# Kernel optimization log

Measured on AMD Instinct MI355X. Metric: run time of the kernel, lower is better.

The kernel has to match this reference:

```python
import jax, jax.numpy as jnp
import numpy as np

B, Hh, Ww, C = 4, 64, 64, 64


def setup_inputs() -> dict:
    key = jax.random.key(0)
    ks = jax.random.split(key, 5)
    scale = 1.0 / np.sqrt(C)
    return {
        "x": jax.random.normal(ks[0], (B, Hh, Ww, C), dtype=jnp.float32),
        "Wq": jax.random.normal(ks[1], (C, C), dtype=jnp.float32) * scale,
        "bq": jnp.zeros((C,), dtype=jnp.float32),
        "Wk": jax.random.normal(ks[2], (C, C), dtype=jnp.float32) * scale,
        "bk": jnp.zeros((C,), dtype=jnp.float32),
        "Wv": jax.random.normal(ks[3], (C, C), dtype=jnp.float32) * scale,
        "bv": jnp.zeros((C,), dtype=jnp.float32),
        "gamma": jax.random.normal(ks[4], (1,), dtype=jnp.float32) * 0.05,
    }


def reference(x, Wq, bq, Wk, bk, Wv, bv, gamma):
    b, h, w, c = x.shape
    n = h * w
    # 1x1 convs == per-pixel dense projections
    q = (jnp.einsum('bhwc,cf->bhwf', x, Wq) + bq).reshape(b, n, c)
    k = (jnp.einsum('bhwc,cf->bhwf', x, Wk) + bk).reshape(b, n, c)
    v = (jnp.einsum('bhwc,cf->bhwf', x, Wv) + bv).reshape(b, n, c)
    # energy[b, i, j] = <q_i, k_j>; no scaling, softmax over last axis (j)
    energy = jnp.einsum('bic,bjc->bij', q, k)
    attn = jax.nn.softmax(energy, axis=-1)
    # original: transpose(matmul(value^T, attention)) -> out[b,n,c] = sum_m attn[b,m,n] * v[b,m,c]
    out = jnp.einsum('bmn,bmc->bnc', attn, v)
    out = out.reshape(b, h, w, c)
    return gamma * out + x
```

## Files before the change

### kernel.cpp

```cpp
#include <hip/hip_runtime.h>
#include <hip/hip_bf16.h>


typedef __attribute__((ext_vector_type(8))) short short8;
typedef __attribute__((ext_vector_type(4))) float f32x4;
typedef __attribute__((ext_vector_type(4))) unsigned int u32x4;
typedef __attribute__((ext_vector_type(2))) unsigned int u32x2;

#define DEV static __device__ __forceinline__

DEV unsigned short f2bf(float f) {
    __hip_bfloat16 h = __float2bfloat16(f);
    return __builtin_bit_cast(unsigned short, h);
}
DEV unsigned int pack2(float lo, float hi) {
    return (unsigned int)f2bf(lo) | ((unsigned int)f2bf(hi) << 16);
}
DEV f32x4 MFMA(short8 a, short8 b, f32x4 c) {
    return __builtin_amdgcn_mfma_f32_16x16x32_bf16(a, b, c, 0, 0, 0);
}

#define OFF_Q    0u
#define OFF_K    2097152u
#define OFF_VT   4194304u
#define OFF_WT   6291456u
#define OFF_S    6316032u
#define OFF_RINV 6381568u

__global__ __launch_bounds__(256) void k0z(const float* __restrict__ Wq,
                                           const float* __restrict__ Wk,
                                           const float* __restrict__ Wv,
                                           unsigned short* __restrict__ wt,
                                           float* __restrict__ sbuf) {
    int e = blockIdx.x * 256 + threadIdx.x;
    sbuf[e] = 0.0f;
    if (e < 3 * 4096) {
        int w3 = e >> 12, rem = e & 4095, f = rem >> 6, c = rem & 63;
        const float* W = (w3 == 0) ? Wq : (w3 == 1) ? Wk : Wv;
        wt[e] = f2bf(W[c * 64 + f]);
    }
}

__global__ __launch_bounds__(256) void k1_proj(const float* __restrict__ x,
                                               const unsigned short* __restrict__ wt,
                                               const float* __restrict__ bq,
                                               const float* __restrict__ bk,
                                               const float* __restrict__ bv,
                                               unsigned short* __restrict__ qg,
                                               unsigned short* __restrict__ kg,
                                               unsigned short* __restrict__ vtg) {
    __shared__ __align__(16) char XT[8192];
    __shared__ __align__(16) char WT[24576];
    __shared__ __align__(16) char VTILE[9216];
    int t = threadIdx.x, blk = blockIdx.x;

    {
        int m = t >> 2, q4 = t & 3;
        const f32x4* xs = (const f32x4*)(x + (size_t)(blk * 64 + m) * 64 + q4 * 16);
        f32x4 fa = xs[0], fbv = xs[1], fc = xs[2], fd = xs[3];
        u32x4 u0 = { pack2(fa[0],fa[1]), pack2(fa[2],fa[3]), pack2(fbv[0],fbv[1]), pack2(fbv[2],fbv[3]) };
        u32x4 u1 = { pack2(fc[0],fc[1]), pack2(fc[2],fc[3]), pack2(fd[0],fd[1]), pack2(fd[2],fd[3]) };
        int sw = (m & 7) << 4;
        *(u32x4*)(XT + m * 128 + ((q4 * 32) ^ sw)) = u0;
        *(u32x4*)(XT + m * 128 + ((q4 * 32 + 16) ^ sw)) = u1;
    }
    for (int w3 = 0; w3 < 3; ++w3) {
        int f = t >> 2, q4 = t & 3;
        const u32x4* s = (const u32x4*)(wt + w3 * 4096 + f * 64 + q4 * 16);
        u32x4 u0 = s[0], u1 = s[1];
        int sw = (f & 7) << 4;
        *(u32x4*)(WT + w3 * 8192 + f * 128 + ((q4 * 32) ^ sw)) = u0;
        *(u32x4*)(WT + w3 * 8192 + f * 128 + ((q4 * 32 + 16) ^ sw)) = u1;
    }
    __syncthreads();

    int lane = t & 63, wid = t >> 6, g = lane >> 4, ln = lane & 15;
    int arow = wid * 16 + ln;
    short8 a0 = *(const short8*)(XT + arow * 128 + ((16 * g) ^ ((arow & 7) << 4)));
    short8 a1 = *(const short8*)(XT + arow * 128 + ((64 + 16 * g) ^ ((arow & 7) << 4)));

    for (int w3 = 0; w3 < 3; ++w3) {
        const char* wtile = WT + w3 * 8192;
        const float* bias = (w3 == 0) ? bq : (w3 == 1) ? bk : bv;
        #pragma unroll
        for (int fb = 0; fb < 4; ++fb) {
            int frow = fb * 16 + ln;
            short8 b0 = *(const short8*)(wtile + frow * 128 + ((16 * g) ^ ((frow & 7) << 4)));
            short8 b1 = *(const short8*)(wtile + frow * 128 + ((64 + 16 * g) ^ ((frow & 7) << 4)));
            f32x4 acc = {0.f, 0.f, 0.f, 0.f};
            acc = MFMA(a0, b0, acc);
            acc = MFMA(a1, b1, acc);
            float bval = bias[frow];
            if (w3 < 2) {
                unsigned short* dst = (w3 == 0) ? qg : kg;
                int gr = blk * 64 + wid * 16 + 4 * g;
                #pragma unroll
                for (int r = 0; r < 4; ++r)
                    dst[(size_t)(gr + r) * 64 + frow] = f2bf(acc[r] + bval);
            } else {
                unsigned short* vt = (unsigned short*)VTILE;
                int mloc = wid * 16 + 4 * g;
                #pragma unroll
                for (int r = 0; r < 4; ++r)
                    vt[frow * 72 + mloc + r] = f2bf(acc[r] + bval);
            }
        }
    }
    __syncthreads();
    {
        int f = t >> 2, mq = t & 3;
        u32x4 u0 = *(const u32x4*)(VTILE + f * 144 + mq * 32);
        u32x4 u1 = *(const u32x4*)(VTILE + f * 144 + mq * 32 + 16);
        int b = blk >> 6, n0 = (blk & 63) * 64;
        unsigned short* dst = vtg + (size_t)b * 262144 + f * 4096 + n0 + mq * 16;
        *(u32x4*)(dst) = u0;
        *(u32x4*)(dst + 8) = u1;
    }
}

__global__ __launch_bounds__(256) void k2_rowsum(const unsigned short* __restrict__ qg,
                                                 const unsigned short* __restrict__ kg,
                                                 float* __restrict__ sbuf) {
    __shared__ __align__(16) char QT[8192];
    __shared__ __align__(16) char KT[8192];
    int t = threadIdx.x, blk = blockIdx.x;
    int b = blk >> 8, ns = (blk >> 6) & 3, mb = blk & 63;
    int m0 = mb * 64, nbase = ns * 1024;
    int row = t >> 2, q4 = t & 3;
    int sw = (row & 7) << 4;

    {
        const u32x4* s = (const u32x4*)(qg + (size_t)(b * 4096 + m0 + row) * 64 + q4 * 16);
        u32x4 u0 = s[0], u1 = s[1];
        *(u32x4*)(QT + row * 128 + ((q4 * 32) ^ sw)) = u0;
        *(u32x4*)(QT + row * 128 + ((q4 * 32 + 16) ^ sw)) = u1;
    }
    u32x4 pf0, pf1;
    {
        const u32x4* ks = (const u32x4*)(kg + (size_t)(b * 4096 + nbase + row) * 64 + q4 * 16);
        pf0 = ks[0]; pf1 = ks[1];
    }
    __syncthreads();

    int lane = t & 63, wid = t >> 6, g = lane >> 4, ln = lane & 15;
    int arow = wid * 16 + ln;
    short8 a0 = *(const short8*)(QT + arow * 128 + ((16 * g) ^ ((arow & 7) << 4)));
    short8 a1 = *(const short8*)(QT + arow * 128 + ((64 + 16 * g) ^ ((arow & 7) << 4)));

    float acc0 = 0.f, acc1 = 0.f, acc2 = 0.f, acc3 = 0.f;
    for (int nc = 0; nc < 16; ++nc) {
        *(u32x4*)(KT + row * 128 + ((q4 * 32) ^ sw)) = pf0;
        *(u32x4*)(KT + row * 128 + ((q4 * 32 + 16) ^ sw)) = pf1;
        __syncthreads();
        if (nc < 15) {
            const u32x4* ks = (const u32x4*)(kg + (size_t)(b * 4096 + nbase + (nc + 1) * 64 + row) * 64 + q4 * 16);
            pf0 = ks[0]; pf1 = ks[1];
        }
        #pragma unroll
        for (int j = 0; j < 4; ++j) {
            int brow = j * 16 + ln;
            short8 b0 = *(const short8*)(KT + brow * 128 + ((16 * g) ^ ((brow & 7) << 4)));
            short8 b1 = *(const short8*)(KT + brow * 128 + ((64 + 16 * g) ^ ((brow & 7) << 4)));
            f32x4 e = {0.f, 0.f, 0.f, 0.f};
            e = MFMA(a0, b0, e);
            e = MFMA(a1, b1, e);
            acc0 += __expf(e[0]); acc1 += __expf(e[1]);
            acc2 += __expf(e[2]); acc3 += __expf(e[3]);
        }
        __syncthreads();
    }
    #pragma unroll
    for (int msk = 1; msk < 16; msk <<= 1) {
        acc0 += __shfl_xor(acc0, msk);
        acc1 += __shfl_xor(acc1, msk);
        acc2 += __shfl_xor(acc2, msk);
        acc3 += __shfl_xor(acc3, msk);
    }
    if (ln == 0) {
        float* base = sbuf + b * 4096 + m0 + wid * 16 + 4 * g;
        unsafeAtomicAdd(base + 0, acc0);
        unsafeAtomicAdd(base + 1, acc1);
        unsafeAtomicAdd(base + 2, acc2);
        unsafeAtomicAdd(base + 3, acc3);
    }
}

__global__ __launch_bounds__(256) void r2_init(const float* __restrict__ sbuf,
                                               float* __restrict__ rinv,
                                               const float* __restrict__ x,
                                               float* __restrict__ outp) {
    int tid = blockIdx.x * 256 + threadIdx.x;
    if (tid < 16384) rinv[tid] = 1.0f / sbuf[tid];
    f32x4 v = *(const f32x4*)(x + 4 * (size_t)tid);
    *(f32x4*)(outp + 4 * (size_t)tid) = v;
}

__global__ __launch_bounds__(256) void k3_out(const unsigned short* __restrict__ qg,
                                              const unsigned short* __restrict__ kg,
                                              const unsigned short* __restrict__ vtg,
                                              const float* __restrict__ rinv,
                                              const float* __restrict__ gamma,
                                              float* __restrict__ outp) {
    __shared__ __align__(16) char KT[8192];
    __shared__ __align__(16) char QT[8192];
    __shared__ __align__(16) char VT[8192];
    __shared__ __align__(16) char PL[8192];
    int t = threadIdx.x, blk = blockIdx.x;
    int b = blk >> 8, ms = (blk >> 6) & 3, nb = blk & 63;
    int n0 = nb * 64, mbase = ms * 1024;
    int row = t >> 2, q4 = t & 3;
    int sw = (row & 7) << 4;

    {
        const u32x4* s = (const u32x4*)(kg + (size_t)(b * 4096 + n0 + row) * 64 + q4 * 16);
        u32x4 u0 = s[0], u1 = s[1];
        *(u32x4*)(KT + row * 128 + ((q4 * 32) ^ sw)) = u0;
        *(u32x4*)(KT + row * 128 + ((q4 * 32 + 16) ^ sw)) = u1;
    }
    u32x4 qpf0, qpf1, vpf0, vpf1;
    {
        const u32x4* qs = (const u32x4*)(qg + (size_t)(b * 4096 + mbase + row) * 64 + q4 * 16);
        qpf0 = qs[0]; qpf1 = qs[1];
        const unsigned short* vs = vtg + (size_t)b * 262144 + row * 4096 + mbase + q4 * 16;
        vpf0 = *(const u32x4*)(vs);
        vpf1 = *(const u32x4*)(vs + 8);
    }
    __syncthreads();

    int lane = t & 63, wid = t >> 6, g = lane >> 4, ln = lane & 15;
    int krow = wid * 16 + ln;
    short8 kb0 = *(const short8*)(KT + krow * 128 + ((16 * g) ^ ((krow & 7) << 4)));
    short8 kb1 = *(const short8*)(KT + krow * 128 + ((64 + 16 * g) ^ ((krow & 7) << 4)));

    f32x4 z = {0.f, 0.f, 0.f, 0.f};
    f32x4 oacc[4] = {z, z, z, z};
    char* pbase = PL + wid * 2048;
    int psw = (ln & 7) << 4;
    const float* rblk = rinv + b * 4096 + mbase;

    for (int mc = 0; mc < 16; ++mc) {
        {
            *(u32x4*)(QT + row * 128 + ((q4 * 32) ^ sw)) = qpf0;
            *(u32x4*)(QT + row * 128 + ((q4 * 32 + 16) ^ sw)) = qpf1;
            *(u32x4*)(VT + row * 128 + ((q4 * 32) ^ sw)) = vpf0;
            *(u32x4*)(VT + row * 128 + ((q4 * 32 + 16) ^ sw)) = vpf1;
        }
        __syncthreads();
        if (mc < 15) {
            int m1 = mbase + (mc + 1) * 64;
            const u32x4* qs = (const u32x4*)(qg + (size_t)(b * 4096 + m1 + row) * 64 + q4 * 16);
            qpf0 = qs[0]; qpf1 = qs[1];
            const unsigned short* vs = vtg + (size_t)b * 262144 + row * 4096 + m1 + q4 * 16;
            vpf0 = *(const u32x4*)(vs);
            vpf1 = *(const u32x4*)(vs + 8);
        }
        const float* rp = rblk + mc * 64;
        #pragma unroll
        for (int s = 0; s < 4; ++s) {
            int qrow = 16 * s + ln;
            int qsw = (qrow & 7) << 4;
            short8 as0 = *(const short8*)(QT + qrow * 128 + ((16 * g) ^ qsw));
            short8 as1 = *(const short8*)(QT + qrow * 128 + ((64 + 16 * g) ^ qsw));
            f32x4 e = {0.f, 0.f, 0.f, 0.f};
            e = MFMA(as0, kb0, e);
            e = MFMA(as1, kb1, e);
            f32x4 rv = *(const f32x4*)(rp + 16 * s + 4 * g);
            float p0 = __expf(e[0]) * rv[0];
            float p1 = __expf(e[1]) * rv[1];
            float p2 = __expf(e[2]) * rv[2];
            float p3 = __expf(e[3]) * rv[3];
            u32x2 pu = { pack2(p0, p1), pack2(p2, p3) };
            *(u32x2*)(pbase + ln * 128 + ((32 * s + 8 * g) ^ psw)) = pu;
        }
        short8 pa0 = *(const short8*)(pbase + ln * 128 + ((16 * g) ^ psw));
        short8 pa1 = *(const short8*)(pbase + ln * 128 + ((64 + 16 * g) ^ psw));
        #pragma unroll
        for (int fb = 0; fb < 4; ++fb) {
            int crow = fb * 16 + ln;
            int csw = (crow & 7) << 4;
            short8 vb0 = *(const short8*)(VT + crow * 128 + ((16 * g) ^ csw));
            short8 vb1 = *(const short8*)(VT + crow * 128 + ((64 + 16 * g) ^ csw));
            oacc[fb] = MFMA(pa0, vb0, oacc[fb]);
            oacc[fb] = MFMA(pa1, vb1, oacc[fb]);
        }
        __syncthreads();
    }

    float gm = gamma[0];
    int nrow = b * 4096 + n0 + wid * 16 + 4 * g;
    #pragma unroll
    for (int fb = 0; fb < 4; ++fb) {
        #pragma unroll
        for (int r = 0; r < 4; ++r) {
            int idx = (nrow + r) * 64 + fb * 16 + ln;
            unsafeAtomicAdd(outp + idx, gm * oacc[fb][r]);
        }
    }
}

extern "C" void kernel_launch(void* const* d_in, const int* in_sizes, int n_in,
                              void* d_out, int out_size, void* d_ws, size_t ws_size,
                              hipStream_t stream) {
    const float* x  = (const float*)d_in[0];
    const float* Wq = (const float*)d_in[1];
    const float* bq = (const float*)d_in[2];
    const float* Wk = (const float*)d_in[3];
    const float* bk = (const float*)d_in[4];
    const float* Wv = (const float*)d_in[5];
    const float* bv = (const float*)d_in[6];
    const float* gm = (const float*)d_in[7];
    char* ws = (char*)d_ws;
    float* outp = (float*)d_out;

    unsigned short* qg  = (unsigned short*)(ws + OFF_Q);
    unsigned short* kg  = (unsigned short*)(ws + OFF_K);
    unsigned short* vtg = (unsigned short*)(ws + OFF_VT);
    unsigned short* wt  = (unsigned short*)(ws + OFF_WT);
    float* sbuf         = (float*)(ws + OFF_S);
    float* rinv         = (float*)(ws + OFF_RINV);

    k0z<<<64, 256, 0, stream>>>(Wq, Wk, Wv, wt, sbuf);
    k1_proj<<<256, 256, 0, stream>>>(x, wt, bq, bk, bv, qg, kg, vtg);
    k2_rowsum<<<1024, 256, 0, stream>>>(qg, kg, sbuf);
    r2_init<<<1024, 256, 0, stream>>>(sbuf, rinv, x, outp);
    k3_out<<<1024, 256, 0, stream>>>(qg, kg, vtg, rinv, gm, outp);
}
```

Baseline: 136.3 us.

## Fold log2e into Q, use exp2 with log-normalizer bias, restructure attention kernels

Folds log2(e) into the Q weights and bias, so the softmax exponentials become native exp2. The reciprocal row sum becomes a -log2 term that seeds the MFMA accumulator, which removes the per-element multiply. The projection kernel is split across three times as many blocks, one per weight matrix. The rowsum and output kernels get finer m/n splits, double-buffered smaller LDS tiles and occupancy hints. The output kernel also switches the P·V product to 16x16x16 MFMA fed straight from registers instead of an LDS round trip. The risks are more atomic-add traffic from twice as many blocks, more loop iterations with barriers, and bf16 precision changes from folding the scale into Q.

```diff
diff --git a/kernel.cpp b/kernel.cpp
--- a/kernel.cpp
+++ b/kernel.cpp
@@ -3,11 +3,13 @@
 
 
 typedef __attribute__((ext_vector_type(8))) short short8;
+typedef __attribute__((ext_vector_type(4))) short short4b;
 typedef __attribute__((ext_vector_type(4))) float f32x4;
 typedef __attribute__((ext_vector_type(4))) unsigned int u32x4;
 typedef __attribute__((ext_vector_type(2))) unsigned int u32x2;
 
 #define DEV static __device__ __forceinline__
+#define LOG2E 1.4426950408889634f
 
 DEV unsigned short f2bf(float f) {
     __hip_bfloat16 h = __float2bfloat16(f);
@@ -16,8 +18,26 @@
 DEV unsigned int pack2(float lo, float hi) {
     return (unsigned int)f2bf(lo) | ((unsigned int)f2bf(hi) << 16);
 }
-DEV f32x4 MFMA(short8 a, short8 b, f32x4 c) {
+DEV f32x4 MFMA32(short8 a, short8 b, f32x4 c) {
     return __builtin_amdgcn_mfma_f32_16x16x32_bf16(a, b, c, 0, 0, 0);
+}
+DEV f32x4 MFMA16(short4b a, short4b b, f32x4 c) {
+#if __has_builtin(__builtin_amdgcn_mfma_f32_16x16x16_bf16)
+    return __builtin_amdgcn_mfma_f32_16x16x16_bf16(a, b, c, 0, 0, 0);
+#elif __has_builtin(__builtin_amdgcn_mfma_f32_16x16x16bf16_1k)
+    return __builtin_amdgcn_mfma_f32_16x16x16bf16_1k(a, b, c, 0, 0, 0);
+#else
+    f32x4 d = c;
+    asm volatile("v_mfma_f32_16x16x16_bf16 %0, %1, %2, %0" : "+v"(d) : "v"(a), "v"(b));
+    return d;
+#endif
+}
+DEV float EXP2(float x) {
+#if __has_builtin(__builtin_amdgcn_exp2f)
+    return __builtin_amdgcn_exp2f(x);
+#else
+    return exp2f(x);
+#endif
 }
 
 #define OFF_Q    0u
@@ -25,7 +45,7 @@
 #define OFF_VT   4194304u
 #define OFF_WT   6291456u
 #define OFF_S    6316032u
-#define OFF_RINV 6381568u
+#define OFF_LR   6381568u
 
 __global__ __launch_bounds__(256) void k0z(const float* __restrict__ Wq,
                                            const float* __restrict__ Wk,
@@ -37,7 +57,8 @@
     if (e < 3 * 4096) {
         int w3 = e >> 12, rem = e & 4095, f = rem >> 6, c = rem & 63;
         const float* W = (w3 == 0) ? Wq : (w3 == 1) ? Wk : Wv;
-        wt[e] = f2bf(W[c * 64 + f]);
+        float s = (w3 == 0) ? LOG2E : 1.0f;
+        wt[e] = f2bf(W[c * 64 + f] * s);
     }
 }
 
@@ -50,27 +71,28 @@
                                                unsigned short* __restrict__ kg,
                                                unsigned short* __restrict__ vtg) {
     __shared__ __align__(16) char XT[8192];
-    __shared__ __align__(16) char WT[24576];
+    __shared__ __align__(16) char WT1[8192];
     __shared__ __align__(16) char VTILE[9216];
     int t = threadIdx.x, blk = blockIdx.x;
+    int w3 = blk >> 8, rb = blk & 255;
 
     {
         int m = t >> 2, q4 = t & 3;
-        const f32x4* xs = (const f32x4*)(x + (size_t)(blk * 64 + m) * 64 + q4 * 16);
-        f32x4 fa = xs[0], fbv = xs[1], fc = xs[2], fd = xs[3];
-        u32x4 u0 = { pack2(fa[0],fa[1]), pack2(fa[2],fa[3]), pack2(fbv[0],fbv[1]), pack2(fbv[2],fbv[3]) };
+        const f32x4* xs = (const f32x4*)(x + (size_t)(rb * 64 + m) * 64 + q4 * 16);
+        f32x4 fa = xs[0], f2 = xs[1], fc = xs[2], fd = xs[3];
+        u32x4 u0 = { pack2(fa[0],fa[1]), pack2(fa[2],fa[3]), pack2(f2[0],f2[1]), pack2(f2[2],f2[3]) };
         u32x4 u1 = { pack2(fc[0],fc[1]), pack2(fc[2],fc[3]), pack2(fd[0],fd[1]), pack2(fd[2],fd[3]) };
         int sw = (m & 7) << 4;
         *(u32x4*)(XT + m * 128 + ((q4 * 32) ^ sw)) = u0;
         *(u32x4*)(XT + m * 128 + ((q4 * 32 + 16) ^ sw)) = u1;
     }
-    for (int w3 = 0; w3 < 3; ++w3) {
+    {
         int f = t >> 2, q4 = t & 3;
         const u32x4* s = (const u32x4*)(wt + w3 * 4096 + f * 64 + q4 * 16);
         u32x4 u0 = s[0], u1 = s[1];
         int sw = (f & 7) << 4;
-        *(u32x4*)(WT + w3 * 8192 + f * 128 + ((q4 * 32) ^ sw)) = u0;
-        *(u32x4*)(WT + w3 * 8192 + f * 128 + ((q4 * 32 + 16) ^ sw)) = u1;
+        *(u32x4*)(WT1 + f * 128 + ((q4 * 32) ^ sw)) = u0;
+        *(u32x4*)(WT1 + f * 128 + ((q4 * 32 + 16) ^ sw)) = u1;
     }
     __syncthreads();
 
@@ -78,67 +100,65 @@
     int arow = wid * 16 + ln;
     short8 a0 = *(const short8*)(XT + arow * 128 + ((16 * g) ^ ((arow & 7) << 4)));
     short8 a1 = *(const short8*)(XT + arow * 128 + ((64 + 16 * g) ^ ((arow & 7) << 4)));
-
-    for (int w3 = 0; w3 < 3; ++w3) {
-        const char* wtile = WT + w3 * 8192;
-        const float* bias = (w3 == 0) ? bq : (w3 == 1) ? bk : bv;
-        #pragma unroll
-        for (int fb = 0; fb < 4; ++fb) {
-            int frow = fb * 16 + ln;
-            short8 b0 = *(const short8*)(wtile + frow * 128 + ((16 * g) ^ ((frow & 7) << 4)));
-            short8 b1 = *(const short8*)(wtile + frow * 128 + ((64 + 16 * g) ^ ((frow & 7) << 4)));
-            f32x4 acc = {0.f, 0.f, 0.f, 0.f};
-            acc = MFMA(a0, b0, acc);
-            acc = MFMA(a1, b1, acc);
-            float bval = bias[frow];
-            if (w3 < 2) {
-                unsigned short* dst = (w3 == 0) ? qg : kg;
-                int gr = blk * 64 + wid * 16 + 4 * g;
-                #pragma unroll
-                for (int r = 0; r < 4; ++r)
-                    dst[(size_t)(gr + r) * 64 + frow] = f2bf(acc[r] + bval);
-            } else {
-                unsigned short* vt = (unsigned short*)VTILE;
-                int mloc = wid * 16 + 4 * g;
-                #pragma unroll
-                for (int r = 0; r < 4; ++r)
-                    vt[frow * 72 + mloc + r] = f2bf(acc[r] + bval);
-            }
-        }
-    }
-    __syncthreads();
-    {
+    const float* bias = (w3 == 0) ? bq : (w3 == 1) ? bk : bv;
+    float bscale = (w3 == 0) ? LOG2E : 1.0f;
+
+    #pragma unroll
+    for (int fb = 0; fb < 4; ++fb) {
+        int frow = fb * 16 + ln;
+        short8 b0 = *(const short8*)(WT1 + frow * 128 + ((16 * g) ^ ((frow & 7) << 4)));
+        short8 b1 = *(const short8*)(WT1 + frow * 128 + ((64 + 16 * g) ^ ((frow & 7) << 4)));
+        f32x4 acc = {0.f, 0.f, 0.f, 0.f};
+        acc = MFMA32(a0, b0, acc);
+        acc = MFMA32(a1, b1, acc);
+        float bval = bias[frow] * bscale;
+        if (w3 < 2) {
+            unsigned short* dst = (w3 == 0) ? qg : kg;
+            int gr = rb * 64 + wid * 16 + 4 * g;
+            #pragma unroll
+            for (int r = 0; r < 4; ++r)
+                dst[(size_t)(gr + r) * 64 + frow] = f2bf(acc[r] + bval);
+        } else {
+            unsigned short* vt = (unsigned short*)VTILE;
+            int mloc = wid * 16 + 4 * g;
+            #pragma unroll
+            for (int r = 0; r < 4; ++r)
+                vt[frow * 72 + mloc + r] = f2bf(acc[r] + bval);
+        }
+    }
+    if (w3 == 2) {
+        __syncthreads();
         int f = t >> 2, mq = t & 3;
         u32x4 u0 = *(const u32x4*)(VTILE + f * 144 + mq * 32);
         u32x4 u1 = *(const u32x4*)(VTILE + f * 144 + mq * 32 + 16);
-        int b = blk >> 6, n0 = (blk & 63) * 64;
+        int b = rb >> 6, n0 = (rb & 63) * 64;
         unsigned short* dst = vtg + (size_t)b * 262144 + f * 4096 + n0 + mq * 16;
         *(u32x4*)(dst) = u0;
         *(u32x4*)(dst + 8) = u1;
     }
 }
 
-__global__ __launch_bounds__(256) void k2_rowsum(const unsigned short* __restrict__ qg,
-                                                 const unsigned short* __restrict__ kg,
-                                                 float* __restrict__ sbuf) {
+__global__ __launch_bounds__(256, 8) void k2_rowsum(const unsigned short* __restrict__ qg,
+                                                    const unsigned short* __restrict__ kg,
+                                                    float* __restrict__ sbuf) {
     __shared__ __align__(16) char QT[8192];
-    __shared__ __align__(16) char KT[8192];
+    __shared__ __align__(16) char KT2[2][4096];
     int t = threadIdx.x, blk = blockIdx.x;
-    int b = blk >> 8, ns = (blk >> 6) & 3, mb = blk & 63;
-    int m0 = mb * 64, nbase = ns * 1024;
-    int row = t >> 2, q4 = t & 3;
-    int sw = (row & 7) << 4;
-
-    {
+    int b = blk >> 9, ns = (blk >> 6) & 7, mb = blk & 63;
+    int m0 = mb * 64, nbase = ns * 512;
+
+    {
+        int row = t >> 2, q4 = t & 3, sw = (row & 7) << 4;
         const u32x4* s = (const u32x4*)(qg + (size_t)(b * 4096 + m0 + row) * 64 + q4 * 16);
         u32x4 u0 = s[0], u1 = s[1];
         *(u32x4*)(QT + row * 128 + ((q4 * 32) ^ sw)) = u0;
         *(u32x4*)(QT + row * 128 + ((q4 * 32 + 16) ^ sw)) = u1;
     }
-    u32x4 pf0, pf1;
-    {
-        const u32x4* ks = (const u32x4*)(kg + (size_t)(b * 4096 + nbase + row) * 64 + q4 * 16);
-        pf0 = ks[0]; pf1 = ks[1];
+    int srow = t >> 3, sb = t & 7, ssw = (srow & 7) << 4;
+    const unsigned short* kbase = kg + (size_t)(b * 4096 + nbase) * 64;
+    {
+        u32x4 u = *(const u32x4*)(kbase + srow * 64 + sb * 8);
+        *(u32x4*)(KT2[0] + srow * 128 + ((sb * 16) ^ ssw)) = u;
     }
     __syncthreads();
 
@@ -148,26 +168,27 @@
     short8 a1 = *(const short8*)(QT + arow * 128 + ((64 + 16 * g) ^ ((arow & 7) << 4)));
 
     float acc0 = 0.f, acc1 = 0.f, acc2 = 0.f, acc3 = 0.f;
+    int buf = 0;
+    u32x4 pf;
     for (int nc = 0; nc < 16; ++nc) {
-        *(u32x4*)(KT + row * 128 + ((q4 * 32) ^ sw)) = pf0;
-        *(u32x4*)(KT + row * 128 + ((q4 * 32 + 16) ^ sw)) = pf1;
+        if (nc < 15)
+            pf = *(const u32x4*)(kbase + (size_t)((nc + 1) * 32 + srow) * 64 + sb * 8);
+        const char* kt = KT2[buf];
+        #pragma unroll
+        for (int j = 0; j < 2; ++j) {
+            int brow = j * 16 + ln, bsw = (brow & 7) << 4;
+            short8 kb0 = *(const short8*)(kt + brow * 128 + ((16 * g) ^ bsw));
+            short8 kb1 = *(const short8*)(kt + brow * 128 + ((64 + 16 * g) ^ bsw));
+            f32x4 e = {0.f, 0.f, 0.f, 0.f};
+            e = MFMA32(a0, kb0, e);
+            e = MFMA32(a1, kb1, e);
+            acc0 += EXP2(e[0]); acc1 += EXP2(e[1]);
+            acc2 += EXP2(e[2]); acc3 += EXP2(e[3]);
+        }
+        if (nc < 15)
+            *(u32x4*)(KT2[buf ^ 1] + srow * 128 + ((sb * 16) ^ ssw)) = pf;
         __syncthreads();
-        if (nc < 15) {
-            const u32x4* ks = (const u32x4*)(kg + (size_t)(b * 4096 + nbase + (nc + 1) * 64 + row) * 64 + q4 * 16);
-            pf0 = ks[0]; pf1 = ks[1];
-        }
-        #pragma unroll
-        for (int j = 0; j < 4; ++j) {
-            int brow = j * 16 + ln;
-            short8 b0 = *(const short8*)(KT + brow * 128 + ((16 * g) ^ ((brow & 7) << 4)));
-            short8 b1 = *(const short8*)(KT + brow * 128 + ((64 + 16 * g) ^ ((brow & 7) << 4)));
-            f32x4 e = {0.f, 0.f, 0.f, 0.f};
-            e = MFMA(a0, b0, e);
-            e = MFMA(a1, b1, e);
-            acc0 += __expf(e[0]); acc1 += __expf(e[1]);
-            acc2 += __expf(e[2]); acc3 += __expf(e[3]);
-        }
-        __syncthreads();
+        buf ^= 1;
     }
     #pragma unroll
     for (int msk = 1; msk < 16; msk <<= 1) {
@@ -186,115 +207,97 @@
 }
 
 __global__ __launch_bounds__(256) void r2_init(const float* __restrict__ sbuf,
-                                               float* __restrict__ rinv,
+                                               float* __restrict__ lrbuf,
                                                const float* __restrict__ x,
                                                float* __restrict__ outp) {
     int tid = blockIdx.x * 256 + threadIdx.x;
-    if (tid < 16384) rinv[tid] = 1.0f / sbuf[tid];
+    if (tid < 16384) lrbuf[tid] = -__log2f(sbuf[tid]);
     f32x4 v = *(const f32x4*)(x + 4 * (size_t)tid);
     *(f32x4*)(outp + 4 * (size_t)tid) = v;
 }
 
-__global__ __launch_bounds__(256) void k3_out(const unsigned short* __restrict__ qg,
-                                              const unsigned short* __restrict__ kg,
-                                              const unsigned short* __restrict__ vtg,
-                                              const float* __restrict__ rinv,
-                                              const float* __restrict__ gamma,
-                                              float* __restrict__ outp) {
+__global__ __launch_bounds__(256, 8) void k3_out(const unsigned short* __restrict__ qg,
+                                                 const unsigned short* __restrict__ kg,
+                                                 const unsigned short* __restrict__ vtg,
+                                                 const float* __restrict__ lrbuf,
+                                                 const float* __restrict__ gamma,
+                                                 float* __restrict__ outp) {
     __shared__ __align__(16) char KT[8192];
-    __shared__ __align__(16) char QT[8192];
-    __shared__ __align__(16) char VT[8192];
-    __shared__ __align__(16) char PL[8192];
+    __shared__ __align__(16) char QT2[2][2048];
+    __shared__ __align__(16) char VT2[2][2560];
     int t = threadIdx.x, blk = blockIdx.x;
-    int b = blk >> 8, ms = (blk >> 6) & 3, nb = blk & 63;
-    int n0 = nb * 64, mbase = ms * 1024;
-    int row = t >> 2, q4 = t & 3;
-    int sw = (row & 7) << 4;
-
-    {
+    int b = blk >> 9, ms = (blk >> 6) & 7, nb = blk & 63;
+    int n0 = nb * 64, mbase = ms * 512;
+
+    {
+        int row = t >> 2, q4 = t & 3, sw = (row & 7) << 4;
         const u32x4* s = (const u32x4*)(kg + (size_t)(b * 4096 + n0 + row) * 64 + q4 * 16);
         u32x4 u0 = s[0], u1 = s[1];
         *(u32x4*)(KT + row * 128 + ((q4 * 32) ^ sw)) = u0;
         *(u32x4*)(KT + row * 128 + ((q4 * 32 + 16) ^ sw)) = u1;
     }
-    u32x4 qpf0, qpf1, vpf0, vpf1;
-    {
-        const u32x4* qs = (const u32x4*)(qg + (size_t)(b * 4096 + mbase + row) * 64 + q4 * 16);
-        qpf0 = qs[0]; qpf1 = qs[1];
-        const unsigned short* vs = vtg + (size_t)b * 262144 + row * 4096 + mbase + q4 * 16;
-        vpf0 = *(const u32x4*)(vs);
-        vpf1 = *(const u32x4*)(vs + 8);
-    }
+    int qrow = t >> 4, qh = t & 15;
+    int vc = t >> 2, vq = t & 3;
+    int qssw = (qrow & 7) << 4;
+    const unsigned short* qbase = qg + (size_t)(b * 4096 + mbase) * 64;
+    const unsigned short* vbase = vtg + (size_t)b * 262144 + (size_t)vc * 4096 + mbase;
+    {
+        u32x2 qu = *(const u32x2*)(qbase + qrow * 64 + qh * 4);
+        *(u32x2*)(QT2[0] + qrow * 128 + ((qh * 8) ^ qssw)) = qu;
+        u32x2 vu = *(const u32x2*)(vbase + vq * 4);
+        *(u32x2*)(VT2[0] + vc * 40 + vq * 8) = vu;
+    }
+    int lane = t & 63, wid = t >> 6, g = lane >> 4, ln = lane & 15;
+    const float* lrb = lrbuf + b * 4096 + mbase + 4 * g;
+    f32x4 lcur = *(const f32x4*)(lrb);
     __syncthreads();
 
-    int lane = t & 63, wid = t >> 6, g = lane >> 4, ln = lane & 15;
-    int krow = wid * 16 + ln;
-    short8 kb0 = *(const short8*)(KT + krow * 128 + ((16 * g) ^ ((krow & 7) << 4)));
-    short8 kb1 = *(const short8*)(KT + krow * 128 + ((64 + 16 * g) ^ ((krow & 7) << 4)));
+    int krow = wid * 16 + ln, ksw = (krow & 7) << 4;
+    short8 kb0 = *(const short8*)(KT + krow * 128 + ((16 * g) ^ ksw));
+    short8 kb1 = *(const short8*)(KT + krow * 128 + ((64 + 16 * g) ^ ksw));
 
     f32x4 z = {0.f, 0.f, 0.f, 0.f};
     f32x4 oacc[4] = {z, z, z, z};
-    char* pbase = PL + wid * 2048;
-    int psw = (ln & 7) << 4;
-    const float* rblk = rinv + b * 4096 + mbase;
-
-    for (int mc = 0; mc < 16; ++mc) {
-        {
-            *(u32x4*)(QT + row * 128 + ((q4 * 32) ^ sw)) = qpf0;
-            *(u32x4*)(QT + row * 128 + ((q4 * 32 + 16) ^ sw)) = qpf1;
-            *(u32x4*)(VT + row * 128 + ((q4 * 32) ^ sw)) = vpf0;
-            *(u32x4*)(VT + row * 128 + ((q4 * 32 + 16) ^ sw)) = vpf1;
-        }
-        __syncthreads();
-        if (mc < 15) {
-            int m1 = mbase + (mc + 1) * 64;
-            const u32x4* qs = (const u32x4*)(qg + (size_t)(b * 4096 + m1 + row) * 64 + q4 * 16);
-            qpf0 = qs[0]; qpf1 = qs[1];
-            const unsigned short* vs = vtg + (size_t)b * 262144 + row * 4096 + m1 + q4 * 16;
-            vpf0 = *(const u32x4*)(vs);
-            vpf1 = *(const u32x4*)(vs + 8);
-        }
-        const float* rp = rblk + mc * 64;
-        #pragma unroll
-        for (int s = 0; s < 4; ++s) {
-            int qrow = 16 * s + ln;
-            int qsw = (qrow & 7) << 4;
-            short8 as0 = *(const short8*)(QT + qrow * 128 + ((16 * g) ^ qsw));
-            short8 as1 = *(const short8*)(QT + qrow * 128 + ((64 + 16 * g) ^ qsw));
-            f32x4 e = {0.f, 0.f, 0.f, 0.f};
-            e = MFMA(as0, kb0, e);
-            e = MFMA(as1, kb1, e);
-            f32x4 rv = *(const f32x4*)(rp + 16 * s + 4 * g);
-            float p0 = __expf(e[0]) * rv[0];
-            float p1 = __expf(e[1]) * rv[1];
-            float p2 = __expf(e[2]) * rv[2];
-            float p3 = __expf(e[3]) * rv[3];
-            u32x2 pu = { pack2(p0, p1), pack2(p2, p3) };
-            *(u32x2*)(pbase + ln * 128 + ((32 * s + 8 * g) ^ psw)) = pu;
-        }
-        short8 pa0 = *(const short8*)(pbase + ln * 128 + ((16 * g) ^ psw));
-        short8 pa1 = *(const short8*)(pbase + ln * 128 + ((64 + 16 * g) ^ psw));
+    int qsw = (ln & 7) << 4;
+    int buf = 0;
+    u32x2 qpf, vpf;
+    f32x4 lnext;
+
+    for (int mc = 0; mc < 32; ++mc) {
+        if (mc < 31) {
+            qpf = *(const u32x2*)(qbase + (size_t)((mc + 1) * 16 + qrow) * 64 + qh * 4);
+            vpf = *(const u32x2*)(vbase + (mc + 1) * 16 + vq * 4);
+            lnext = *(const f32x4*)(lrb + (mc + 1) * 16);
+        }
+        const char* qt = QT2[buf];
+        const char* vt = VT2[buf];
+        short8 as0 = *(const short8*)(qt + ln * 128 + ((16 * g) ^ qsw));
+        short8 as1 = *(const short8*)(qt + ln * 128 + ((64 + 16 * g) ^ qsw));
+        f32x4 e = MFMA32(as1, kb1, MFMA32(as0, kb0, lcur));
+        float p0 = EXP2(e[0]), p1 = EXP2(e[1]), p2 = EXP2(e[2]), p3 = EXP2(e[3]);
+        u32x2 pw = { pack2(p0, p1), pack2(p2, p3) };
+        short4b pa = __builtin_bit_cast(short4b, pw);
         #pragma unroll
         for (int fb = 0; fb < 4; ++fb) {
-            int crow = fb * 16 + ln;
-            int csw = (crow & 7) << 4;
-            short8 vb0 = *(const short8*)(VT + crow * 128 + ((16 * g) ^ csw));
-            short8 vb1 = *(const short8*)(VT + crow * 128 + ((64 + 16 * g) ^ csw));
-            oacc[fb] = MFMA(pa0, vb0, oacc[fb]);
-            oacc[fb] = MFMA(pa1, vb1, oacc[fb]);
+            short4b vb = *(const short4b*)(vt + (fb * 16 + ln) * 40 + g * 8);
+            oacc[fb] = MFMA16(pa, vb, oacc[fb]);
+        }
+        if (mc < 31) {
+            *(u32x2*)(QT2[buf ^ 1] + qrow * 128 + ((qh * 8) ^ qssw)) = qpf;
+            *(u32x2*)(VT2[buf ^ 1] + vc * 40 + vq * 8) = vpf;
+            lcur = lnext;
         }
         __syncthreads();
+        buf ^= 1;
     }
 
     float gm = gamma[0];
-    int nrow = b * 4096 + n0 + wid * 16 + 4 * g;
+    int nr = b * 4096 + n0 + wid * 16 + 4 * g;
     #pragma unroll
     for (int fb = 0; fb < 4; ++fb) {
         #pragma unroll
-        for (int r = 0; r < 4; ++r) {
-            int idx = (nrow + r) * 64 + fb * 16 + ln;
-            unsafeAtomicAdd(outp + idx, gm * oacc[fb][r]);
-        }
+        for (int r = 0; r < 4; ++r)
+            unsafeAtomicAdd(outp + (size_t)(nr + r) * 64 + fb * 16 + ln, gm * oacc[fb][r]);
     }
 }
 
@@ -317,11 +320,11 @@
     unsigned short* vtg = (unsigned short*)(ws + OFF_VT);
     unsigned short* wt  = (unsigned short*)(ws + OFF_WT);
     float* sbuf         = (float*)(ws + OFF_S);
-    float* rinv         = (float*)(ws + OFF_RINV);
+    float* lrbuf        = (float*)(ws + OFF_LR);
 
     k0z<<<64, 256, 0, stream>>>(Wq, Wk, Wv, wt, sbuf);
-    k1_proj<<<256, 256, 0, stream>>>(x, wt, bq, bk, bv, qg, kg, vtg);
-    k2_rowsum<<<1024, 256, 0, stream>>>(qg, kg, sbuf);
-    r2_init<<<1024, 256, 0, stream>>>(sbuf, rinv, x, outp);
-    k3_out<<<1024, 256, 0, stream>>>(qg, kg, vtg, rinv, gm, outp);
-}
+    k1_proj<<<768, 256, 0, stream>>>(x, wt, bq, bk, bv, qg, kg, vtg);
+    k2_rowsum<<<2048, 256, 0, stream>>>(qg, kg, sbuf);
+    r2_init<<<1024, 256, 0, stream>>>(sbuf, lrbuf, x, outp);
+    k3_out<<<2048, 256, 0, stream>>>(qg, kg, vtg, lrbuf, gm, outp);
+}
```

New measurement: 141.2 us. +3.6%, slower.
